# Kernel tuning notes

Hardware: AMD Instinct MI355X
Metric: run time of the kernel (lower is better)

Reference implementation:

```python
import jax, jax.numpy as jnp
import numpy as np
from jax import lax

B, C, L = 2048, 9605, 8
WL_PER_LABEL = 50
ALPHA = 0.5        # training_config['alpha4']
ALPHA1 = 0.1       # margin
ALPHA2 = 2.0       # training_config['alpha2']
ALPHA3 = 10.0      # training_config['alpha3']
ALPHA_OTHER = 0.5
NEG = jnp.float32(-1e30)


def setup_inputs() -> dict:
    key = jax.random.key(0)
    k1, k2, k3, k4 = jax.random.split(key, 4)
    x = jax.random.normal(k1, (B, C), dtype=jnp.float32) * 2.0
    y = (jax.random.uniform(k2, (B, C)) < 0.005).astype(jnp.float32)
    y_neg = (jax.random.uniform(k3, (B, C)) < 0.005).astype(jnp.float32)
    # whitelist masks: L app-labels, each whitelisting ~WL_PER_LABEL raw classes
    idx = jax.random.randint(k4, (L, WL_PER_LABEL), 0, C)
    wl_masks = jnp.zeros((L, C), dtype=bool).at[jnp.arange(L)[:, None], idx].set(True)
    return {"x": x, "y": y, "y_neg": y_neg, "wl_masks": wl_masks}


def reference(x, y, y_neg, wl_masks):
    # y_neg is consumed by the original forward (find_gt_whitelist) but never
    # affects the returned loss, faithfully ignored here.
    xs_pos = jax.nn.sigmoid(x)                                  # [B, C]
    # top_k_thres = max(11th-largest sigmoid, alpha_other)
    thres = jnp.maximum(lax.top_k(xs_pos, 11)[0][:, 10], ALPHA_OTHER)  # [B]
    # per-label whitelist max: m[b,l] = max_{c in wl_l} xs_pos[b,c]
    m = jnp.max(jnp.where(wl_masks[None, :, :], xs_pos[:, None, :], NEG), axis=-1)  # [B, L]
    # label l is a ground-truth whitelist label iff y has any positive in wl_l
    has_pos = jnp.einsum('bc,lc->bl', y, wl_masks.astype(y.dtype)) > 0   # [B, L]
    correct_max = jnp.max(jnp.where(has_pos, m, NEG), axis=-1)           # [B]
    incorrect_max = jnp.max(jnp.where(~has_pos, m, NEG), axis=-1)        # [B]
    any_correct = jnp.any(has_pos, axis=-1)
    any_incorrect = jnp.any(~has_pos, axis=-1)
    # union whitelist max (the "other" branch uses xs_pos over all wl indices)
    union_max = jnp.max(jnp.where(jnp.any(wl_masks, axis=0)[None, :], xs_pos, NEG), axis=-1)
    x1 = jnp.where(any_correct, correct_max, thres)
    x2 = jnp.where(any_correct,
                   jnp.where(any_incorrect, jnp.maximum(incorrect_max, thres), thres),
                   union_max)
    coef = jnp.where(any_correct, 1.0, 1.0 - ALPHA)
    d = x2 - x1 + ALPHA1
    rank = jnp.where(d > 0, ALPHA2, 1.0) * jax.nn.sigmoid(ALPHA3 * d)
    return jnp.mean(coef * rank)
```

## Files before the change

### kernel.cpp

```cpp
#include <hip/hip_runtime.h>

#define CC 9605
#define BB 2048
#define LL 8
#define CAND_MAX 384
#define NEGF (-1e30f)

#define WS_PARTIALS_OFF 16384

__device__ __forceinline__ unsigned enc_f(float f) {
  unsigned u = __float_as_uint(f);
  return (u & 0x80000000u) ? ~u : (u | 0x80000000u);
}
__device__ __forceinline__ float dec_u(unsigned e) {
  unsigned u = (e & 0x80000000u) ? (e & 0x7fffffffu) : ~e;
  return __uint_as_float(u);
}
__device__ __forceinline__ float sigm(float z) {
  return 1.0f / (1.0f + __expf(-z));
}

__global__ void wl_sniff(const unsigned* __restrict__ wlw,
                         unsigned* __restrict__ wsu) {
  const int nwords = (LL * CC) / 4;
  const int stride = gridDim.x * blockDim.x;
  unsigned f = 0u;
  for (int j = blockIdx.x * blockDim.x + threadIdx.x; j < nwords; j += stride) {
    unsigned w = wlw[j];
#pragma unroll
    for (int k = 0; k < 4; ++k) {
      unsigned b = (w >> (8 * k)) & 255u;
      if (b == 1u)    { f |= 2u; if (k != 0) f |= 1u; }
      if (b == 0x3fu) { f |= 8u; if (k == 1) f |= 4u; }
    }
  }
#pragma unroll
  for (int off = 32; off >= 1; off >>= 1) f |= __shfl_xor(f, off, 64);
  if ((threadIdx.x & 63) == 0 && f) atomicOr(&wsu[1], f);
}

__global__ void wl_compact(const unsigned char* __restrict__ wl,
                           unsigned* __restrict__ wsu) {
  const int tid = threadIdx.x;
  const int lane = tid & 63;
  const int c = blockIdx.x * 256 + tid;
  const unsigned g = wsu[1];
  const int dt = (g & 1u) ? 0 : (g & 4u) ? 3 : (g & 2u) ? 1 : (g & 8u) ? 2 : 0;
  const int* wl32 = (const int*)wl;
  const float* wlf = (const float*)wl;
  const unsigned short* wlh = (const unsigned short*)wl;
  unsigned m = 0u;
  if (c < CC) {
#pragma unroll
    for (int l = 0; l < LL; ++l) {
      int j = l * CC + c;
      bool on;
      if (dt == 0) on = (wl[j] != 0);
      else if (dt == 1) on = (wl32[j] != 0);
      else if (dt == 2) on = (wlf[j] != 0.0f);
      else on = (wlh[j] != 0);
      if (on) m |= (1u << l);
    }
  }
  unsigned long long bal = __ballot(m != 0u);
  if (bal) {
    unsigned wcnt = (unsigned)__popcll(bal);
    unsigned basep = 0u;
    if (lane == 0) basep = atomicAdd(&wsu[0], wcnt);
    basep = __shfl(basep, 0, 64);
    if (m) {
      unsigned pos = basep + (unsigned)__popcll(bal & ((1ull << lane) - 1ull));
      if (pos < 2048u) wsu[4 + pos] = ((unsigned)c << 8) | m;
    }
  }
}

__global__ __launch_bounds__(256, 6) void loss_kernel(
    const float* __restrict__ x, const float* __restrict__ y,
    const unsigned* __restrict__ wsu, float* __restrict__ partials) {
  __shared__ unsigned sh_cand[CAND_MAX];
  __shared__ unsigned sh_redM[4];
  __shared__ unsigned sh_redC[4];
  __shared__ unsigned sh_cnt;
  __shared__ unsigned sh_e11;
  __shared__ float sh_wl[4][10];

  const int tid = threadIdx.x;
  const int lane = tid & 63;
  const int wid = tid >> 6;
  const int b = blockIdx.x;
  const long long base = (long long)b * CC;

  const int soff = (4 - (b & 3)) & 3;
  const int ngroups = (CC - soff) >> 2;
  const int tailn = CC - soff - (ngroups << 2);
  const int m_extra = soff + tailn;
  const float4* vp = (const float4*)(x + base + soff);
  float4 t[10];
#pragma unroll
  for (int i = 0; i < 9; ++i) t[i] = vp[tid + (i << 8)];
  const int g9 = tid + (9 << 8);
  const bool v9 = (g9 < ngroups);
  if (v9) t[9] = vp[g9];
  float tailv = 0.0f;
  const bool has_tail = (tid < m_extra);
  if (has_tail) {
    int tailcol = (tid < soff) ? tid : (soff + (ngroups << 2) + (tid - soff));
    tailv = x[base + tailcol];
  }

  const unsigned nu = wsu[0];
  const unsigned* ents = wsu + 4;
  unsigned ent0 = 0u, ent1 = 0u;
  float gx0 = NEGF, gy0 = 0.0f, gx1 = NEGF, gy1 = 0.0f;
  const bool h0 = (unsigned)tid < nu;
  const bool h1 = (unsigned)(tid + 256) < nu;
  if (h0) ent0 = ents[tid];
  if (h1) ent1 = ents[tid + 256];
  if (h0) { gx0 = x[base + (ent0 >> 8)]; gy0 = y[base + (ent0 >> 8)]; }
  if (h1) { gx1 = x[base + (ent1 >> 8)]; gy1 = y[base + (ent1 >> 8)]; }

  uint4 u[10];
  unsigned mx = 0u;
#pragma unroll
  for (int i = 0; i < 9; ++i) {
    u[i].x = enc_f(t[i].x); u[i].y = enc_f(t[i].y);
    u[i].z = enc_f(t[i].z); u[i].w = enc_f(t[i].w);
    mx = max(mx, max(max(u[i].x, u[i].y), max(u[i].z, u[i].w)));
  }
  if (v9) {
    u[9].x = enc_f(t[9].x); u[9].y = enc_f(t[9].y);
    u[9].z = enc_f(t[9].z); u[9].w = enc_f(t[9].w);
    mx = max(mx, max(max(u[9].x, u[9].y), max(u[9].z, u[9].w)));
  } else {
    u[9].x = 0u; u[9].y = 0u; u[9].z = 0u; u[9].w = 0u;
  }
  unsigned et = 0u;
  if (has_tail) { et = enc_f(tailv); mx = max(mx, et); }
  if (tid == 0) sh_cnt = 0u;

#pragma unroll
  for (int off = 32; off >= 1; off >>= 1) mx = max(mx, __shfl_xor(mx, off, 64));
  if (lane == 0) sh_redM[wid] = mx;
  __syncthreads();
  const unsigned Emax =
      max(max(sh_redM[0], sh_redM[1]), max(sh_redM[2], sh_redM[3]));

  auto blk_count = [&](unsigned T) -> unsigned {
    unsigned cnt = 0u;
#pragma unroll
    for (int i = 0; i < 10; ++i) {
      cnt += (u[i].x >= T) + (u[i].y >= T) + (u[i].z >= T) + (u[i].w >= T);
    }
    cnt += (et >= T);
#pragma unroll
    for (int off = 32; off >= 1; off >>= 1) cnt += __shfl_xor(cnt, off, 64);
    __syncthreads();
    if (lane == 0) sh_redC[wid] = cnt;
    __syncthreads();
    return sh_redC[0] + sh_redC[1] + sh_redC[2] + sh_redC[3];
  };

  unsigned E11 = 0u;
  bool done = false;
  unsigned lo = (Emax > (1u << 23)) ? (Emax - (1u << 23)) : 1u;
  unsigned hi = Emax + 1u;
  unsigned c = blk_count(lo);
  while (c < 11u && lo > 1u) {
    hi = lo;
    lo = (lo > (1u << 23)) ? (lo - (1u << 23)) : 1u;
    c = blk_count(lo);
  }
  while (c > CAND_MAX) {
    if (hi - lo <= 1u) { E11 = lo; done = true; break; }
    unsigned mid = lo + ((hi - lo) >> 1);
    unsigned cm = blk_count(mid);
    if (cm >= 11u) { lo = mid; c = cm; } else { hi = mid; }
  }

  if (!done) {
    unsigned nloc = 0u;
#pragma unroll
    for (int i = 0; i < 10; ++i) {
      nloc += (u[i].x >= lo) + (u[i].y >= lo) + (u[i].z >= lo) + (u[i].w >= lo);
    }
    nloc += (et >= lo);
    unsigned scan = nloc;
#pragma unroll
    for (int off = 1; off < 64; off <<= 1) {
      unsigned nn = __shfl_up(scan, off, 64);
      if (lane >= off) scan += nn;
    }
    unsigned wtot = __shfl(scan, 63, 64);
    unsigned basep = 0u;
    if (lane == 0) basep = atomicAdd(&sh_cnt, wtot);
    basep = __shfl(basep, 0, 64);
    unsigned pos = basep + scan - nloc;
#pragma unroll
    for (int i = 0; i < 10; ++i) {
      if (u[i].x >= lo) sh_cand[pos++] = u[i].x;
      if (u[i].y >= lo) sh_cand[pos++] = u[i].y;
      if (u[i].z >= lo) sh_cand[pos++] = u[i].z;
      if (u[i].w >= lo) sh_cand[pos++] = u[i].w;
    }
    if (et >= lo) sh_cand[pos++] = et;
    __syncthreads();

    if (wid == 0) {
      unsigned v0[6];
#pragma unroll
      for (int j = 0; j < 6; ++j) {
        unsigned idx = (unsigned)lane + 64u * j;
        v0[j] = (idx < c) ? sh_cand[idx] : 0u;
      }
      unsigned ans = 0u;
      for (int r = 0; r < 11; ++r) {
        unsigned lmx = v0[0];
#pragma unroll
        for (int j = 1; j < 6; ++j) lmx = max(lmx, v0[j]);
        unsigned wm = lmx;
#pragma unroll
        for (int off = 32; off >= 1; off >>= 1)
          wm = max(wm, __shfl_xor(wm, off, 64));
        ans = wm;
        if (r < 10) {
          unsigned long long bal = __ballot(lmx == wm);
          int first = (int)__ffsll((long long)bal) - 1;
          if (lane == first) {
            bool rm = false;
#pragma unroll
            for (int j = 0; j < 6; ++j) {
              if (!rm && v0[j] == wm) { v0[j] = 0u; rm = true; }
            }
          }
        }
      }
      if (lane == 0) sh_e11 = ans;
    }
    __syncthreads();
    E11 = sh_e11;
  }

  float lm[8];
#pragma unroll
  for (int l = 0; l < 8; ++l) lm[l] = NEGF;
  unsigned pmask = 0u;
  if (h0) {
    unsigned mk = ent0 & 255u;
    pmask |= mk;
    if (gy0 > 0.0f) pmask |= (mk << 8);
#pragma unroll
    for (int l = 0; l < 8; ++l)
      if ((mk >> l) & 1u) lm[l] = fmaxf(lm[l], gx0);
  }
  if (h1) {
    unsigned mk = ent1 & 255u;
    pmask |= mk;
    if (gy1 > 0.0f) pmask |= (mk << 8);
#pragma unroll
    for (int l = 0; l < 8; ++l)
      if ((mk >> l) & 1u) lm[l] = fmaxf(lm[l], gx1);
  }
  for (unsigned e = (unsigned)tid + 512u; e < nu; e += 256u) {
    unsigned ent = ents[e];
    unsigned mk = ent & 255u;
    float xv = x[base + (ent >> 8)];
    float yv = y[base + (ent >> 8)];
    pmask |= mk;
    if (yv > 0.0f) pmask |= (mk << 8);
#pragma unroll
    for (int l = 0; l < 8; ++l)
      if ((mk >> l) & 1u) lm[l] = fmaxf(lm[l], xv);
  }
#pragma unroll
  for (int off = 32; off >= 1; off >>= 1) {
    pmask |= __shfl_xor(pmask, off, 64);
#pragma unroll
    for (int l = 0; l < 8; ++l) lm[l] = fmaxf(lm[l], __shfl_xor(lm[l], off, 64));
  }
  if (lane == 0) {
#pragma unroll
    for (int l = 0; l < 8; ++l) sh_wl[wid][l] = lm[l];
    sh_wl[wid][8] = __uint_as_float(pmask);
  }
  __syncthreads();

  if (tid == 0) {
    float LM[8];
    unsigned PM = 0u;
#pragma unroll
    for (int l = 0; l < 8; ++l) LM[l] = NEGF;
    for (int w = 0; w < 4; ++w) {
#pragma unroll
      for (int l = 0; l < 8; ++l) LM[l] = fmaxf(LM[l], sh_wl[w][l]);
      PM |= __float_as_uint(sh_wl[w][8]);
    }
    unsigned PR = PM & 255u, PO = (PM >> 8) & 255u;
    float thres = fmaxf(sigm(dec_u(E11)), 0.5f);
    float cmax = NEGF, imax = NEGF, umax = NEGF;
#pragma unroll
    for (int l = 0; l < 8; ++l) {
      if ((PR >> l) & 1u) {
        float ml = sigm(LM[l]);
        umax = fmaxf(umax, ml);
        if ((PO >> l) & 1u) cmax = fmaxf(cmax, ml);
        else imax = fmaxf(imax, ml);
      }
    }
    bool anyc = (PO != 0u);
    bool anyi = (PO != 255u);
    float x1 = anyc ? cmax : thres;
    float x2 = anyc ? (anyi ? fmaxf(imax, thres) : thres)
                    : ((nu > 0u) ? umax : NEGF);
    float coef = anyc ? 1.0f : 0.5f;
    float dd = x2 - x1 + 0.1f;
    float rank = ((dd > 0.0f) ? 2.0f : 1.0f) * sigm(10.0f * dd);
    partials[b] = coef * rank;
  }
}

__global__ void final_reduce(const float* __restrict__ partials,
                             float* __restrict__ out) {
  __shared__ float sh[4];
  const int tid = threadIdx.x;
  const int lane = tid & 63;
  const int wid = tid >> 6;
  float s = 0.0f;
  for (int i = tid; i < BB; i += 256) s += partials[i];
#pragma unroll
  for (int off = 32; off >= 1; off >>= 1) s += __shfl_xor(s, off, 64);
  if (lane == 0) sh[wid] = s;
  __syncthreads();
  if (tid == 0) out[0] = (sh[0] + sh[1] + sh[2] + sh[3]) * (1.0f / (float)BB);
}

extern "C" void kernel_launch(void* const* d_in, const int* in_sizes, int n_in,
                              void* d_out, int out_size, void* d_ws,
                              size_t ws_size, hipStream_t stream) {
  const float* x = (const float*)d_in[0];
  const float* y = (const float*)d_in[1];
  const unsigned char* wl = (const unsigned char*)d_in[3];
  float* out = (float*)d_out;
  unsigned* wsu = (unsigned*)d_ws;
  float* partials = (float*)((char*)d_ws + WS_PARTIALS_OFF);

  hipMemsetAsync(d_ws, 0, 16, stream);
  wl_sniff<<<64, 256, 0, stream>>>((const unsigned*)wl, wsu);
  wl_compact<<<(CC + 255) / 256, 256, 0, stream>>>(wl, wsu);
  loss_kernel<<<BB, 256, 0, stream>>>(x, y, wsu, partials);
  final_reduce<<<1, 256, 0, stream>>>(partials, out);
}
```

Baseline: 223.7 us.

## Merge whitelist sniff into compaction and widen loss kernel to 512 threads

Removes the separate dtype-sniff kernel: each compaction block now redundantly scans the whole whitelist mask and reduces the flags through shared memory, saving one launch. The loss kernel moves from 256 to 512 threads per block with half as many float4 registers per thread, so each row is split across eight waves. All reductions are widened accordingly. The aim is less launch overhead and more parallelism and latency hiding per row. The cost is redundant mask reads in every prep block and more block-wide synchronisation per binary-search step.

```diff
diff --git a/kernel.cpp b/kernel.cpp
--- a/kernel.cpp
+++ b/kernel.cpp
@@ -20,35 +20,34 @@
   return 1.0f / (1.0f + __expf(-z));
 }
 
-__global__ void wl_sniff(const unsigned* __restrict__ wlw,
-                         unsigned* __restrict__ wsu) {
-  const int nwords = (LL * CC) / 4;
-  const int stride = gridDim.x * blockDim.x;
-  unsigned f = 0u;
-  for (int j = blockIdx.x * blockDim.x + threadIdx.x; j < nwords; j += stride) {
-    unsigned w = wlw[j];
-#pragma unroll
-    for (int k = 0; k < 4; ++k) {
-      unsigned b = (w >> (8 * k)) & 255u;
-      if (b == 1u)    { f |= 2u; if (k != 0) f |= 1u; }
-      if (b == 0x3fu) { f |= 8u; if (k == 1) f |= 4u; }
-    }
-  }
-#pragma unroll
-  for (int off = 32; off >= 1; off >>= 1) f |= __shfl_xor(f, off, 64);
-  if ((threadIdx.x & 63) == 0 && f) atomicOr(&wsu[1], f);
-}
-
-__global__ void wl_compact(const unsigned char* __restrict__ wl,
-                           unsigned* __restrict__ wsu) {
+__global__ __launch_bounds__(256) void wl_prep(
+    const unsigned char* __restrict__ wl, unsigned* __restrict__ wsu) {
+  __shared__ unsigned sh_f[4];
   const int tid = threadIdx.x;
   const int lane = tid & 63;
-  const int c = blockIdx.x * 256 + tid;
-  const unsigned g = wsu[1];
+  const int wid = tid >> 6;
+  const unsigned* wlw = (const unsigned*)wl;
+  const int nwords = (LL * CC) / 4;
+  unsigned f = 0u;
+  for (int j = tid; j < nwords; j += 256) {
+    unsigned w = wlw[j];
+#pragma unroll
+    for (int k = 0; k < 4; ++k) {
+      unsigned bv = (w >> (8 * k)) & 255u;
+      if (bv == 1u)    { f |= 2u; if (k != 0) f |= 1u; }
+      if (bv == 0x3fu) { f |= 8u; if (k == 1) f |= 4u; }
+    }
+  }
+#pragma unroll
+  for (int off = 32; off >= 1; off >>= 1) f |= __shfl_xor(f, off, 64);
+  if (lane == 0) sh_f[wid] = f;
+  __syncthreads();
+  const unsigned g = sh_f[0] | sh_f[1] | sh_f[2] | sh_f[3];
   const int dt = (g & 1u) ? 0 : (g & 4u) ? 3 : (g & 2u) ? 1 : (g & 8u) ? 2 : 0;
   const int* wl32 = (const int*)wl;
   const float* wlf = (const float*)wl;
   const unsigned short* wlh = (const unsigned short*)wl;
+  const int c = blockIdx.x * 256 + tid;
   unsigned m = 0u;
   if (c < CC) {
 #pragma unroll
@@ -75,15 +74,15 @@
   }
 }
 
-__global__ __launch_bounds__(256, 6) void loss_kernel(
+__global__ __launch_bounds__(512, 8) void loss_kernel(
     const float* __restrict__ x, const float* __restrict__ y,
     const unsigned* __restrict__ wsu, float* __restrict__ partials) {
   __shared__ unsigned sh_cand[CAND_MAX];
-  __shared__ unsigned sh_redM[4];
-  __shared__ unsigned sh_redC[4];
+  __shared__ unsigned sh_redM[8];
+  __shared__ unsigned sh_redC[8];
   __shared__ unsigned sh_cnt;
   __shared__ unsigned sh_e11;
-  __shared__ float sh_wl[4][10];
+  __shared__ float sh_wl[8][10];
 
   const int tid = threadIdx.x;
   const int lane = tid & 63;
@@ -96,12 +95,12 @@
   const int tailn = CC - soff - (ngroups << 2);
   const int m_extra = soff + tailn;
   const float4* vp = (const float4*)(x + base + soff);
-  float4 t[10];
-#pragma unroll
-  for (int i = 0; i < 9; ++i) t[i] = vp[tid + (i << 8)];
-  const int g9 = tid + (9 << 8);
-  const bool v9 = (g9 < ngroups);
-  if (v9) t[9] = vp[g9];
+  float4 t[5];
+#pragma unroll
+  for (int i = 0; i < 4; ++i) t[i] = vp[tid + (i << 9)];
+  const int g4 = tid + (4 << 9);
+  const bool v4 = (g4 < ngroups);
+  if (v4) t[4] = vp[g4];
   float tailv = 0.0f;
   const bool has_tail = (tid < m_extra);
   if (has_tail) {
@@ -109,31 +108,28 @@
     tailv = x[base + tailcol];
   }
 
-  const unsigned nu = wsu[0];
+  const unsigned nu = min(wsu[0], 2048u);
   const unsigned* ents = wsu + 4;
-  unsigned ent0 = 0u, ent1 = 0u;
-  float gx0 = NEGF, gy0 = 0.0f, gx1 = NEGF, gy1 = 0.0f;
+  unsigned ent0 = 0u;
+  float gx0 = NEGF, gy0 = 0.0f;
   const bool h0 = (unsigned)tid < nu;
-  const bool h1 = (unsigned)(tid + 256) < nu;
   if (h0) ent0 = ents[tid];
-  if (h1) ent1 = ents[tid + 256];
   if (h0) { gx0 = x[base + (ent0 >> 8)]; gy0 = y[base + (ent0 >> 8)]; }
-  if (h1) { gx1 = x[base + (ent1 >> 8)]; gy1 = y[base + (ent1 >> 8)]; }
-
-  uint4 u[10];
+
+  uint4 u[5];
   unsigned mx = 0u;
 #pragma unroll
-  for (int i = 0; i < 9; ++i) {
+  for (int i = 0; i < 4; ++i) {
     u[i].x = enc_f(t[i].x); u[i].y = enc_f(t[i].y);
     u[i].z = enc_f(t[i].z); u[i].w = enc_f(t[i].w);
     mx = max(mx, max(max(u[i].x, u[i].y), max(u[i].z, u[i].w)));
   }
-  if (v9) {
-    u[9].x = enc_f(t[9].x); u[9].y = enc_f(t[9].y);
-    u[9].z = enc_f(t[9].z); u[9].w = enc_f(t[9].w);
-    mx = max(mx, max(max(u[9].x, u[9].y), max(u[9].z, u[9].w)));
+  if (v4) {
+    u[4].x = enc_f(t[4].x); u[4].y = enc_f(t[4].y);
+    u[4].z = enc_f(t[4].z); u[4].w = enc_f(t[4].w);
+    mx = max(mx, max(max(u[4].x, u[4].y), max(u[4].z, u[4].w)));
   } else {
-    u[9].x = 0u; u[9].y = 0u; u[9].z = 0u; u[9].w = 0u;
+    u[4].x = 0u; u[4].y = 0u; u[4].z = 0u; u[4].w = 0u;
   }
   unsigned et = 0u;
   if (has_tail) { et = enc_f(tailv); mx = max(mx, et); }
@@ -143,13 +139,14 @@
   for (int off = 32; off >= 1; off >>= 1) mx = max(mx, __shfl_xor(mx, off, 64));
   if (lane == 0) sh_redM[wid] = mx;
   __syncthreads();
-  const unsigned Emax =
-      max(max(sh_redM[0], sh_redM[1]), max(sh_redM[2], sh_redM[3]));
+  unsigned Emax = sh_redM[0];
+#pragma unroll
+  for (int w = 1; w < 8; ++w) Emax = max(Emax, sh_redM[w]);
 
   auto blk_count = [&](unsigned T) -> unsigned {
     unsigned cnt = 0u;
 #pragma unroll
-    for (int i = 0; i < 10; ++i) {
+    for (int i = 0; i < 5; ++i) {
       cnt += (u[i].x >= T) + (u[i].y >= T) + (u[i].z >= T) + (u[i].w >= T);
     }
     cnt += (et >= T);
@@ -158,7 +155,10 @@
     __syncthreads();
     if (lane == 0) sh_redC[wid] = cnt;
     __syncthreads();
-    return sh_redC[0] + sh_redC[1] + sh_redC[2] + sh_redC[3];
+    unsigned s = sh_redC[0];
+#pragma unroll
+    for (int w = 1; w < 8; ++w) s += sh_redC[w];
+    return s;
   };
 
   unsigned E11 = 0u;
@@ -181,7 +181,7 @@
   if (!done) {
     unsigned nloc = 0u;
 #pragma unroll
-    for (int i = 0; i < 10; ++i) {
+    for (int i = 0; i < 5; ++i) {
       nloc += (u[i].x >= lo) + (u[i].y >= lo) + (u[i].z >= lo) + (u[i].w >= lo);
     }
     nloc += (et >= lo);
@@ -197,7 +197,7 @@
     basep = __shfl(basep, 0, 64);
     unsigned pos = basep + scan - nloc;
 #pragma unroll
-    for (int i = 0; i < 10; ++i) {
+    for (int i = 0; i < 5; ++i) {
       if (u[i].x >= lo) sh_cand[pos++] = u[i].x;
       if (u[i].y >= lo) sh_cand[pos++] = u[i].y;
       if (u[i].z >= lo) sh_cand[pos++] = u[i].z;
@@ -253,15 +253,7 @@
     for (int l = 0; l < 8; ++l)
       if ((mk >> l) & 1u) lm[l] = fmaxf(lm[l], gx0);
   }
-  if (h1) {
-    unsigned mk = ent1 & 255u;
-    pmask |= mk;
-    if (gy1 > 0.0f) pmask |= (mk << 8);
-#pragma unroll
-    for (int l = 0; l < 8; ++l)
-      if ((mk >> l) & 1u) lm[l] = fmaxf(lm[l], gx1);
-  }
-  for (unsigned e = (unsigned)tid + 512u; e < nu; e += 256u) {
+  for (unsigned e = (unsigned)tid + 512u; e < nu; e += 512u) {
     unsigned ent = ents[e];
     unsigned mk = ent & 255u;
     float xv = x[base + (ent >> 8)];
@@ -290,7 +282,7 @@
     unsigned PM = 0u;
 #pragma unroll
     for (int l = 0; l < 8; ++l) LM[l] = NEGF;
-    for (int w = 0; w < 4; ++w) {
+    for (int w = 0; w < 8; ++w) {
 #pragma unroll
       for (int l = 0; l < 8; ++l) LM[l] = fmaxf(LM[l], sh_wl[w][l]);
       PM |= __float_as_uint(sh_wl[w][8]);
@@ -345,8 +337,7 @@
   float* partials = (float*)((char*)d_ws + WS_PARTIALS_OFF);
 
   hipMemsetAsync(d_ws, 0, 16, stream);
-  wl_sniff<<<64, 256, 0, stream>>>((const unsigned*)wl, wsu);
-  wl_compact<<<(CC + 255) / 256, 256, 0, stream>>>(wl, wsu);
-  loss_kernel<<<BB, 256, 0, stream>>>(x, y, wsu, partials);
+  wl_prep<<<(CC + 255) / 256, 256, 0, stream>>>(wl, wsu);
+  loss_kernel<<<BB, 512, 0, stream>>>(x, y, wsu, partials);
   final_reduce<<<1, 256, 0, stream>>>(partials, out);
 }
```

After: 239.8 us. +7.2%, slower.
